# Kernel optimization log

Measured on AMD Instinct MI355X. Metric: run time of the kernel, lower is better.

The kernel has to match this reference:

```python
import jax, jax.numpy as jnp
import numpy as np

K = 16          # n_neighbors
DS = 4          # downsampling_rate
EPS = 1e-5      # BatchNorm eps


def fps(pos, n_samples):
    """Farthest point sampling. pos: [N,3] -> [n_samples] int32 indices (start at node 0)."""
    N = pos.shape[0]
    def body(carry, _):
        dists, last = carry
        d = jnp.sum((pos - pos[last]) ** 2, axis=-1)
        dists = jnp.minimum(dists, d)
        nxt = jnp.argmax(dists).astype(jnp.int32)
        return (dists, nxt), nxt
    init = (jnp.full((N,), 1e10, dtype=pos.dtype), jnp.int32(0))
    _, idxs = jax.lax.scan(body, init, None, length=n_samples - 1)
    return jnp.concatenate([jnp.zeros((1,), jnp.int32), idxs])


def knn(pos, k):
    """k nearest neighbors (incl. self). pos: [N,3] -> [N,k] indices."""
    d = jnp.sum((pos[:, None, :] - pos[None, :, :]) ** 2, axis=-1)  # [N,N]
    _, idx = jax.lax.top_k(-d, k)
    return idx


def setup_inputs() -> dict:
    key = jax.random.key(0)
    ks = jax.random.split(key, 8)
    B, N, C = 4, 4096, 64
    sizes = [C + 3, 128, 128]
    inp = {
        "feat": jax.random.normal(ks[0], (B, N, C), jnp.float32),
        "pos": jax.random.normal(ks[1], (B, N, 3), jnp.float32),
    }
    for i in range(2):
        cin, cout = sizes[i], sizes[i + 1]
        inp[f"W{i+1}"] = jax.random.normal(ks[2 + 2 * i], (cout, cin), jnp.float32) / np.float32(np.sqrt(cin))
        inp[f"b{i+1}"] = jnp.zeros((cout,), jnp.float32)
        inp[f"gamma{i+1}"] = jnp.ones((cout,), jnp.float32)
        inp[f"beta{i+1}"] = jnp.zeros((cout,), jnp.float32)
    return inp


def reference(feat, pos, W1, b1, gamma1, beta1, W2, b2, gamma2, beta2):
    B, N, C = feat.shape
    n_samples = N // DS
    # FPS centroids; the torch code selects them via a boolean mask, i.e. ascending node order
    cent = jax.vmap(lambda p: fps(p, n_samples))(pos)          # [B,S]
    cent = jnp.sort(cent, axis=-1)
    # KNN graph per cloud
    nbr = jax.vmap(lambda p: knn(p, K))(pos)                    # [B,N,K]
    nbr_pos = jax.vmap(lambda p, i: p[i])(pos, nbr)             # [B,N,K,3]
    nbr_feat = jax.vmap(lambda f, i: f[i])(feat, nbr)           # [B,N,K,C]
    # RelativePositionMessage: concat(src_pos - dst_pos, src_feat)
    rel = nbr_pos - pos[:, :, None, :]
    h = jnp.concatenate([rel, nbr_feat], axis=-1)               # [B,N,K,C+3]
    # PointNetConv: (1x1 Conv2d -> BatchNorm2d(training stats) -> ReLU) x2, then max over neighbors
    for W, b, g, be in ((W1, b1, gamma1, beta1), (W2, b2, gamma2, beta2)):
        h = jnp.einsum('bnkc,dc->bnkd', h, W) + b
        mu = jnp.mean(h, axis=(0, 1, 2))
        var = jnp.var(h, axis=(0, 1, 2))
        h = (h - mu) * jax.lax.rsqrt(var + EPS) * g + be
        h = jax.nn.relu(h)
    new_feat = jnp.max(h, axis=2)                               # [B,N,Cout]
    # select centroid nodes
    pos_res = jnp.take_along_axis(pos, cent[..., None], axis=1)        # [B,S,3]
    feat_res = jnp.take_along_axis(new_feat, cent[..., None], axis=1)  # [B,S,Cout]
    return pos_res, feat_res
```

## Files before the change

### kernel.cpp

```cpp
#include <hip/hip_runtime.h>

#define NB 4
#define NN 4096
#define NC 64
#define KNB 16
#define NS 1024
#define M1TOT (NB*NN*KNB)
#define EPSBN 1e-5f
#define XROW 68

__device__ __align__(16) int   g_nbr[NB*NN*KNB];
__device__ int   g_cslot[NB*NN];
__device__ float g_sum1[128];
__device__ float g_sq1[128];
__device__ float g_sum2[128];
__device__ float g_sq2[128];
__device__ __align__(16) float g_hmin[NB*NS*128];
__device__ __align__(16) float g_hmax[NB*NS*128];

__global__ __launch_bounds__(256) void kA(const float* __restrict__ pos, float* __restrict__ out)
{
    __shared__ float spx[NN], spy[NN], spz[NN];
    __shared__ float sbv[2][4];
    __shared__ int   sbj[2][4];
    __shared__ int   cnts[256];
    const int blk = blockIdx.x, t = threadIdx.x;

    if (blk >= 68) {
        if (t < 128) { g_sum1[t]=0.f; g_sq1[t]=0.f; g_sum2[t]=0.f; g_sq2[t]=0.f; }
        return;
    }

    if (blk < 4) {
        const int b = blk;
        const float* pb = pos + (size_t)b*NN*3;
        for (int i = t; i < NN; i += 256) { spx[i]=pb[3*i]; spy[i]=pb[3*i+1]; spz[i]=pb[3*i+2]; }
        __syncthreads();
        float rx[16], ry[16], rz[16], rd[16];
        #pragma unroll
        for (int i=0;i<16;i++){ int j=(t<<4)+i; rx[i]=spx[j]; ry[i]=spy[j]; rz[i]=spz[j]; rd[i]=1e10f; }
        unsigned sel = (t==0) ? 1u : 0u;
        float cx = spx[0], cy = spy[0], cz = spz[0];
        const int lane = t & 63, wid = t >> 6;

        for (int it = 0; it < NS-1; ++it) {
            const int par = it & 1;
            float bv = -1.f; int bj = 0;
            #pragma unroll
            for (int i=0;i<16;i++){
                float dx = rx[i]-cx, dy = ry[i]-cy, dz = rz[i]-cz;
                float d = __fadd_rn(__fadd_rn(__fmul_rn(dx,dx),__fmul_rn(dy,dy)),__fmul_rn(dz,dz));
                float nd = fminf(rd[i], d);
                rd[i] = nd;
                if (nd > bv) { bv = nd; bj = (t<<4)+i; }
            }
            #pragma unroll
            for (int m=1;m<64;m<<=1){
                float ov = __shfl_xor(bv, m);
                int   oj = __shfl_xor(bj, m);
                if (ov > bv || (ov == bv && oj < bj)) { bv = ov; bj = oj; }
            }
            if (lane == 0) { sbv[par][wid] = bv; sbj[par][wid] = bj; }
            __syncthreads();
            float v2 = sbv[par][lane & 3];
            int   j2 = sbj[par][lane & 3];
            #pragma unroll
            for (int m=1;m<4;m<<=1){
                float ov = __shfl_xor(v2, m);
                int   oj = __shfl_xor(j2, m);
                if (ov > v2 || (ov == v2 && oj < j2)) { v2 = ov; j2 = oj; }
            }
            cx = spx[j2]; cy = spy[j2]; cz = spz[j2];
            unsigned rel = (unsigned)(j2 - (t<<4));
            if (rel < 16u) sel |= (1u << rel);
        }
        cnts[t] = (int)__popc(sel);
        __syncthreads();
        if (t == 0) { int run = 0; for (int i=0;i<256;i++){ int c = cnts[i]; cnts[i] = run; run += c; } }
        __syncthreads();
        int base = cnts[t];
        #pragma unroll
        for (int i=0;i<16;i++){
            int j = (t<<4)+i;
            if (sel & (1u<<i)) {
                g_cslot[b*NN + j] = base;
                float* po = out + (size_t)((b<<10) + base)*3;
                po[0]=rx[i]; po[1]=ry[i]; po[2]=rz[i];
                base++;
            } else {
                g_cslot[b*NN + j] = -1;
            }
        }
    } else {
        const int kb = blk - 4;
        const int b = kb >> 4;
        const int q = ((kb & 15) << 8) + t;
        const float* pb = pos + (size_t)b*NN*3;
        for (int i = t; i < NN; i += 256) { spx[i]=pb[3*i]; spy[i]=pb[3*i+1]; spz[i]=pb[3*i+2]; }
        __syncthreads();
        const float qx = spx[q], qy = spy[q], qz = spz[q];
        float bd[16]; int bi[16];
        #pragma unroll
        for (int u=0;u<16;u++){ bd[u]=3e38f; bi[u]=0; }
        float wmax = 3e38f;
        for (int j = 0; j < NN; ++j) {
            float dx = spx[j]-qx, dy = spy[j]-qy, dz = spz[j]-qz;
            float d = __fadd_rn(__fadd_rn(__fmul_rn(dx,dx),__fmul_rn(dy,dy)),__fmul_rn(dz,dz));
            if (d < wmax) {
                float m0 = bd[0]; int mj = 0;
                #pragma unroll
                for (int u=1;u<16;u++){ if (bd[u] > m0) { m0 = bd[u]; mj = u; } }
                #pragma unroll
                for (int u=0;u<16;u++){ if (u == mj) { bd[u] = d; bi[u] = j; } }
                wmax = bd[0];
                #pragma unroll
                for (int u=1;u<16;u++) wmax = fmaxf(wmax, bd[u]);
            }
        }
        int* dst = g_nbr + ((size_t)(b*NN + q) << 4);
        #pragma unroll
        for (int u=0;u<16;u++) dst[u] = bi[u];
    }
}

__device__ __forceinline__ void stage_gemm1(const float* __restrict__ feat, const float* __restrict__ pos,
                                            const float* __restrict__ W1,
                                            float* __restrict__ xls, float* __restrict__ wls,
                                            int b, int nb, int t, float acc[4][8])
{
    for (int i = t; i < 128*67; i += 256) {
        int co = i / 67, ci = i - co*67;
        int row = (ci < 3) ? (64 + ci) : (ci - 3);
        wls[row*128 + co] = W1[i];
    }
    {
        const int s = t >> 2, h = t & 3;
        const int n = nb + (s >> 4), k = s & 15;
        const int gq = b*NN + n;
        const int idx = g_nbr[(gq << 4) + k];
        const float* fr = feat + ((size_t)(b*NN + idx) << 6) + (h << 4);
        float* xr = xls + s*XROW + (h << 4);
        #pragma unroll
        for (int u=0;u<4;u++) ((float4*)xr)[u] = ((const float4*)fr)[u];
        if (h == 0) {
            const float* pn = pos + (size_t)gq*3;
            const float* pi = pos + (size_t)(b*NN + idx)*3;
            xls[s*XROW + 64] = pi[0]-pn[0];
            xls[s*XROW + 65] = pi[1]-pn[1];
            xls[s*XROW + 66] = pi[2]-pn[2];
        }
    }
    __syncthreads();
    const int cg = t & 15, sg = t >> 4;
    #pragma unroll
    for (int r=0;r<4;r++)
        #pragma unroll
        for (int c=0;c<8;c++) acc[r][c] = 0.f;
    for (int i = 0; i < 67; ++i) {
        float4 wa = *(const float4*)&wls[i*128 + (cg<<3)];
        float4 wb = *(const float4*)&wls[i*128 + (cg<<3) + 4];
        #pragma unroll
        for (int r=0;r<4;r++){
            float xv = xls[(sg + (r<<4))*XROW + i];
            acc[r][0] = fmaf(xv, wa.x, acc[r][0]);
            acc[r][1] = fmaf(xv, wa.y, acc[r][1]);
            acc[r][2] = fmaf(xv, wa.z, acc[r][2]);
            acc[r][3] = fmaf(xv, wa.w, acc[r][3]);
            acc[r][4] = fmaf(xv, wb.x, acc[r][4]);
            acc[r][5] = fmaf(xv, wb.y, acc[r][5]);
            acc[r][6] = fmaf(xv, wb.z, acc[r][6]);
            acc[r][7] = fmaf(xv, wb.w, acc[r][7]);
        }
    }
}

__global__ __launch_bounds__(256) void kStats1(const float* __restrict__ feat, const float* __restrict__ pos,
                                               const float* __restrict__ W1, const float* __restrict__ b1)
{
    __shared__ __align__(16) float xls[64*XROW];
    __shared__ __align__(16) float wls[67*128];
    __shared__ float redS4[512], redQ4[512];
    const int t = threadIdx.x, blk = blockIdx.x;
    const int b = blk >> 10, nb = (blk & 1023) << 2;
    float acc[4][8];
    stage_gemm1(feat, pos, W1, xls, wls, b, nb, t, acc);
    const int cg = t & 15, sg = t >> 4, w = sg >> 2;
    #pragma unroll
    for (int c=0;c<8;c++){
        const int ch = (cg<<3)+c;
        const float bb = b1[ch];
        float ls=0.f, lq=0.f;
        #pragma unroll
        for (int r=0;r<4;r++){ float h1 = acc[r][c] + bb; ls += h1; lq = fmaf(h1,h1,lq); }
        ls += __shfl_xor(ls,16); ls += __shfl_xor(ls,32);
        lq += __shfl_xor(lq,16); lq += __shfl_xor(lq,32);
        if ((sg & 3) == 0) { redS4[w*128 + ch] = ls; redQ4[w*128 + ch] = lq; }
    }
    __syncthreads();
    if (t < 128) {
        float s = redS4[t] + redS4[128+t] + redS4[256+t] + redS4[384+t];
        float q = redQ4[t] + redQ4[128+t] + redQ4[256+t] + redQ4[384+t];
        atomicAdd(&g_sum1[t], s);
        atomicAdd(&g_sq1[t], q);
    }
}

__global__ __launch_bounds__(256) void kPassB(const float* __restrict__ feat, const float* __restrict__ pos,
        const float* __restrict__ W1, const float* __restrict__ b1,
        const float* __restrict__ gamma1, const float* __restrict__ beta1,
        const float* __restrict__ W2, const float* __restrict__ b2)
{
    __shared__ __align__(16) float SB[12928];
    __shared__ float scs[128], shs[128];
    __shared__ float redS4[512], redQ4[512];
    const int t = threadIdx.x, blk = blockIdx.x;
    const int b = blk >> 10, nb = (blk & 1023) << 2;
    if (t < 128) {
        const float inv = 1.f/(float)M1TOT;
        float mu  = g_sum1[t]*inv;
        float var = g_sq1[t]*inv - mu*mu;
        float sc  = gamma1[t]*rsqrtf(var + EPSBN);
        scs[t] = sc; shs[t] = beta1[t] - mu*sc;
    }
    float acc[4][8];
    stage_gemm1(feat, pos, W1, SB, SB + 64*XROW, b, nb, t, acc);
    const int cg = t & 15, sg = t >> 4, w = sg >> 2;
    __syncthreads();
    #pragma unroll
    for (int c=0;c<8;c++){
        const int ch = (cg<<3)+c;
        const float bb = b1[ch], sc = scs[ch], sh = shs[ch];
        #pragma unroll
        for (int r=0;r<4;r++){
            float yv = fmaxf(0.f, fmaf(acc[r][c] + bb, sc, sh));
            SB[(sg + (r<<4))*133 + ch] = yv;
        }
    }
    __syncthreads();
    float acc2[4][8];
    #pragma unroll
    for (int r=0;r<4;r++)
        #pragma unroll
        for (int c=0;c<8;c++) acc2[r][c]=0.f;
    for (int kc = 0; kc < 4; ++kc) {
        for (int e = t; e < 4096; e += 256) {
            int dd = e >> 5, kk = e & 31;
            SB[8512 + kk*128 + dd] = W2[(dd << 7) + (kc<<5) + kk];
        }
        __syncthreads();
        for (int kk = 0; kk < 32; ++kk) {
            float4 wa = *(const float4*)&SB[8512 + (kk<<7) + (cg<<3)];
            float4 wb = *(const float4*)&SB[8512 + (kk<<7) + (cg<<3) + 4];
            const int kabs = (kc<<5) + kk;
            #pragma unroll
            for (int r=0;r<4;r++){
                float yv = SB[((sg<<2) + r)*133 + kabs];
                acc2[r][0] = fmaf(yv, wa.x, acc2[r][0]);
                acc2[r][1] = fmaf(yv, wa.y, acc2[r][1]);
                acc2[r][2] = fmaf(yv, wa.z, acc2[r][2]);
                acc2[r][3] = fmaf(yv, wa.w, acc2[r][3]);
                acc2[r][4] = fmaf(yv, wb.x, acc2[r][4]);
                acc2[r][5] = fmaf(yv, wb.y, acc2[r][5]);
                acc2[r][6] = fmaf(yv, wb.z, acc2[r][6]);
                acc2[r][7] = fmaf(yv, wb.w, acc2[r][7]);
            }
        }
        __syncthreads();
    }
    #pragma unroll
    for (int c=0;c<8;c++){
        const int ch = (cg<<3)+c;
        const float bb = b2[ch];
        float ls=0.f, lq=0.f, mn=3e38f, mx=-3e38f;
        #pragma unroll
        for (int r=0;r<4;r++){
            float h2 = acc2[r][c] + bb;
            ls += h2; lq = fmaf(h2,h2,lq);
            mn = fminf(mn,h2); mx = fmaxf(mx,h2);
        }
        ls += __shfl_xor(ls,16); ls += __shfl_xor(ls,32);
        lq += __shfl_xor(lq,16); lq += __shfl_xor(lq,32);
        if ((sg & 3) == 0) { redS4[w*128 + ch] = ls; redQ4[w*128 + ch] = lq; }
        float o;
        o = __shfl_xor(mn,16); mn = fminf(mn,o);
        o = __shfl_xor(mn,32); mn = fminf(mn,o);
        o = __shfl_xor(mx,16); mx = fmaxf(mx,o);
        o = __shfl_xor(mx,32); mx = fmaxf(mx,o);
        if ((sg & 3) == 0) {
            const int node = nb + (sg >> 2);
            const int slot = g_cslot[b*NN + node];
            if (slot >= 0) {
                const int oo = (((b<<10)+slot)<<7) + ch;
                g_hmin[oo] = mn; g_hmax[oo] = mx;
            }
        }
    }
    __syncthreads();
    if (t < 128) {
        float s = redS4[t] + redS4[128+t] + redS4[256+t] + redS4[384+t];
        float q = redQ4[t] + redQ4[128+t] + redQ4[256+t] + redQ4[384+t];
        atomicAdd(&g_sum2[t], s);
        atomicAdd(&g_sq2[t], q);
    }
}

__global__ __launch_bounds__(256) void kFinal(const float* __restrict__ gamma2, const float* __restrict__ beta2,
                                              float* __restrict__ out)
{
    const int gid = blockIdx.x*256 + threadIdx.x;
    const int base = gid << 2;
    const int ch0 = base & 127;
    const float inv = 1.f/(float)M1TOT;
    float4 mx = *(const float4*)&g_hmax[base];
    float4 mn = *(const float4*)&g_hmin[base];
    float4 o;
    {
        float mu = g_sum2[ch0]*inv, var = g_sq2[ch0]*inv - mu*mu;
        float sc = gamma2[ch0]*rsqrtf(var+EPSBN), sh = beta2[ch0] - mu*sc;
        o.x = fmaxf(0.f, fmaf((sc >= 0.f) ? mx.x : mn.x, sc, sh));
    }
    {
        int ch = ch0+1;
        float mu = g_sum2[ch]*inv, var = g_sq2[ch]*inv - mu*mu;
        float sc = gamma2[ch]*rsqrtf(var+EPSBN), sh = beta2[ch] - mu*sc;
        o.y = fmaxf(0.f, fmaf((sc >= 0.f) ? mx.y : mn.y, sc, sh));
    }
    {
        int ch = ch0+2;
        float mu = g_sum2[ch]*inv, var = g_sq2[ch]*inv - mu*mu;
        float sc = gamma2[ch]*rsqrtf(var+EPSBN), sh = beta2[ch] - mu*sc;
        o.z = fmaxf(0.f, fmaf((sc >= 0.f) ? mx.z : mn.z, sc, sh));
    }
    {
        int ch = ch0+3;
        float mu = g_sum2[ch]*inv, var = g_sq2[ch]*inv - mu*mu;
        float sc = gamma2[ch]*rsqrtf(var+EPSBN), sh = beta2[ch] - mu*sc;
        o.w = fmaxf(0.f, fmaf((sc >= 0.f) ? mx.w : mn.w, sc, sh));
    }
    *(float4*)&out[12288 + base] = o;
}

extern "C" void kernel_launch(void* const* d_in, const int* in_sizes, int n_in,
                              void* d_out, int out_size, void* d_ws, size_t ws_size,
                              hipStream_t stream)
{
    (void)in_sizes; (void)n_in; (void)d_ws; (void)ws_size; (void)out_size;
    const float* feat = (const float*)d_in[0];
    const float* pos  = (const float*)d_in[1];
    const float* W1   = (const float*)d_in[2];
    const float* b1   = (const float*)d_in[3];
    const float* g1   = (const float*)d_in[4];
    const float* be1  = (const float*)d_in[5];
    const float* W2   = (const float*)d_in[6];
    const float* b2   = (const float*)d_in[7];
    const float* g2   = (const float*)d_in[8];
    const float* be2  = (const float*)d_in[9];
    float* out = (float*)d_out;

    kA<<<dim3(69),   dim3(256), 0, stream>>>(pos, out);
    kStats1<<<dim3(4096), dim3(256), 0, stream>>>(feat, pos, W1, b1);
    kPassB<<<dim3(4096),  dim3(256), 0, stream>>>(feat, pos, W1, b1, g1, be1, W2, b2);
    kFinal<<<dim3(512),   dim3(256), 0, stream>>>(g2, be2, out);
}
```

Measured before the change: 1.783 ms.

## Split FPS across kernels to overlap with GEMM stages and store h1

Farthest point sampling is split into three chunks whose state is kept in global memory, and each chunk runs in four extra blocks of the KNN kernel and the two GEMM kernels, so the serial FPS loop overlaps with other work. The first-layer activations are written to a large global buffer (g_h1) so the second pass reads them back instead of redoing the gather and GEMM1. Per-node min and max are now stored for every node and picked by centroid index in the final kernel. FPS and KNN use packed float2 math, KNN handles two queries per thread, and the GEMM weights are laid out for float4 loads. The cost is much more global memory traffic for h1 and the per-node min/max, plus a few long-running FPS blocks inside the GEMM grids.

```diff
diff --git a/kernel.cpp b/kernel.cpp
--- a/kernel.cpp
+++ b/kernel.cpp
@@ -1,242 +1,346 @@
 #include <hip/hip_runtime.h>
+
+typedef float f2 __attribute__((ext_vector_type(2)));
 
 #define NB 4
 #define NN 4096
-#define NC 64
 #define KNB 16
 #define NS 1024
 #define M1TOT (NB*NN*KNB)
 #define EPSBN 1e-5f
-#define XROW 68
-
+#define FPS_E0 255
+#define FPS_E1 639
+
+__device__ __align__(16) float g_h1[M1TOT*128];
 __device__ __align__(16) int   g_nbr[NB*NN*KNB];
-__device__ int   g_cslot[NB*NN];
-__device__ float g_sum1[128];
-__device__ float g_sq1[128];
-__device__ float g_sum2[128];
-__device__ float g_sq2[128];
-__device__ __align__(16) float g_hmin[NB*NS*128];
-__device__ __align__(16) float g_hmax[NB*NS*128];
-
-__global__ __launch_bounds__(256) void kA(const float* __restrict__ pos, float* __restrict__ out)
-{
-    __shared__ float spx[NN], spy[NN], spz[NN];
-    __shared__ float sbv[2][4];
-    __shared__ int   sbj[2][4];
-    __shared__ int   cnts[256];
-    const int blk = blockIdx.x, t = threadIdx.x;
-
-    if (blk >= 68) {
-        if (t < 128) { g_sum1[t]=0.f; g_sq1[t]=0.f; g_sum2[t]=0.f; g_sq2[t]=0.f; }
-        return;
-    }
-
-    if (blk < 4) {
-        const int b = blk;
-        const float* pb = pos + (size_t)b*NN*3;
-        for (int i = t; i < NN; i += 256) { spx[i]=pb[3*i]; spy[i]=pb[3*i+1]; spz[i]=pb[3*i+2]; }
+__device__ __align__(16) float g_fps_rd[NB][NN];
+__device__ unsigned g_fps_sel[NB][256];
+__device__ int   g_fps_last[NB];
+__device__ int   g_cent[NB][NS];
+__device__ float g_sum1[128], g_sq1[128], g_sum2[128], g_sq2[128];
+__device__ __align__(16) float g_hminN[NB*NN*128];
+__device__ __align__(16) float g_hmaxN[NB*NN*128];
+
+struct __align__(16) FpsSm {
+    float spx[NN], spy[NN], spz[NN];
+    float sv[2][4]; int sj[2][4];
+    int   cnts[256];
+};
+struct __align__(16) G1Sm {
+    float  xls[64*68];
+    float4 wlsA[68*16], wlsB[68*16];
+    float  redS[512], redQ[512];
+};
+struct __align__(16) G2Sm {
+    float  yls[64*132];
+    float4 w2A[32*16], w2B[32*16];
+    float  scs[128], shs[128];
+    float  redS[512], redQ[512];
+};
+
+__device__ __forceinline__ void fps_chunk(const float* __restrict__ pos, float* __restrict__ out,
+                                          FpsSm* sm, int b, int t, int it0, int it1,
+                                          bool first, bool last)
+{
+#pragma clang fp contract(off)
+    const float* pb = pos + b*NN*3;
+    for (int i = t; i < NN; i += 256) { sm->spx[i]=pb[3*i]; sm->spy[i]=pb[3*i+1]; sm->spz[i]=pb[3*i+2]; }
+    __syncthreads();
+    f2 rx[8], ry[8], rz[8], rd[8];
+    #pragma unroll
+    for (int p=0;p<8;p++){
+        int j = (t<<4) + 2*p;
+        rx[p] = (f2){sm->spx[j], sm->spx[j+1]};
+        ry[p] = (f2){sm->spy[j], sm->spy[j+1]};
+        rz[p] = (f2){sm->spz[j], sm->spz[j+1]};
+    }
+    unsigned sel; int j2;
+    if (first) {
+        #pragma unroll
+        for (int p=0;p<8;p++) rd[p] = (f2){1e10f, 1e10f};
+        sel = (t==0) ? 1u : 0u;
+        j2 = 0;
+    } else {
+        #pragma unroll
+        for (int u=0;u<4;u++){
+            float4 ld = *(const float4*)&g_fps_rd[b][(t<<4)+(u<<2)];
+            rd[2*u]   = (f2){ld.x, ld.y};
+            rd[2*u+1] = (f2){ld.z, ld.w};
+        }
+        sel = g_fps_sel[b][t];
+        j2  = g_fps_last[b];
+    }
+    float cx = sm->spx[j2], cy = sm->spy[j2], cz = sm->spz[j2];
+    const int lane = t & 63, wid = t >> 6;
+
+    for (int it = it0; it < it1; ++it) {
+        const int par = it & 1;
+        f2 c2x = {cx,cx}, c2y = {cy,cy}, c2z = {cz,cz};
+        f2 bv2 = {-1.f,-1.f};
+        #pragma unroll
+        for (int p=0;p<8;p++){
+            f2 dx = rx[p]-c2x, dy = ry[p]-c2y, dz = rz[p]-c2z;
+            f2 m0 = dx*dx, m1 = dy*dy, m2 = dz*dz;
+            f2 a0 = m0 + m1;
+            f2 d  = a0 + m2;
+            rd[p] = __builtin_elementwise_min(rd[p], d);
+            bv2   = __builtin_elementwise_max(bv2, rd[p]);
+        }
+        float bv = fmaxf(bv2.x, bv2.y);
+        int bj = 0;
+        #pragma unroll
+        for (int p=7;p>=0;p--){
+            bj = (rd[p].y == bv) ? ((t<<4)+2*p+1) : bj;
+            bj = (rd[p].x == bv) ? ((t<<4)+2*p)   : bj;
+        }
+        #pragma unroll
+        for (int m=1;m<64;m<<=1){
+            float ov = __shfl_xor(bv, m);
+            int   oj = __shfl_xor(bj, m);
+            if (ov > bv || (ov == bv && oj < bj)) { bv = ov; bj = oj; }
+        }
+        if (lane == 0) { sm->sv[par][wid] = bv; sm->sj[par][wid] = bj; }
         __syncthreads();
-        float rx[16], ry[16], rz[16], rd[16];
-        #pragma unroll
-        for (int i=0;i<16;i++){ int j=(t<<4)+i; rx[i]=spx[j]; ry[i]=spy[j]; rz[i]=spz[j]; rd[i]=1e10f; }
-        unsigned sel = (t==0) ? 1u : 0u;
-        float cx = spx[0], cy = spy[0], cz = spz[0];
-        const int lane = t & 63, wid = t >> 6;
-
-        for (int it = 0; it < NS-1; ++it) {
-            const int par = it & 1;
-            float bv = -1.f; int bj = 0;
-            #pragma unroll
-            for (int i=0;i<16;i++){
-                float dx = rx[i]-cx, dy = ry[i]-cy, dz = rz[i]-cz;
-                float d = __fadd_rn(__fadd_rn(__fmul_rn(dx,dx),__fmul_rn(dy,dy)),__fmul_rn(dz,dz));
-                float nd = fminf(rd[i], d);
-                rd[i] = nd;
-                if (nd > bv) { bv = nd; bj = (t<<4)+i; }
-            }
-            #pragma unroll
-            for (int m=1;m<64;m<<=1){
-                float ov = __shfl_xor(bv, m);
-                int   oj = __shfl_xor(bj, m);
-                if (ov > bv || (ov == bv && oj < bj)) { bv = ov; bj = oj; }
-            }
-            if (lane == 0) { sbv[par][wid] = bv; sbj[par][wid] = bj; }
-            __syncthreads();
-            float v2 = sbv[par][lane & 3];
-            int   j2 = sbj[par][lane & 3];
-            #pragma unroll
-            for (int m=1;m<4;m<<=1){
-                float ov = __shfl_xor(v2, m);
-                int   oj = __shfl_xor(j2, m);
-                if (ov > v2 || (ov == v2 && oj < j2)) { v2 = ov; j2 = oj; }
-            }
-            cx = spx[j2]; cy = spy[j2]; cz = spz[j2];
-            unsigned rel = (unsigned)(j2 - (t<<4));
-            if (rel < 16u) sel |= (1u << rel);
-        }
-        cnts[t] = (int)__popc(sel);
+        float v = sm->sv[par][0]; int jn = sm->sj[par][0];
+        #pragma unroll
+        for (int w=1;w<4;w++){
+            float ov = sm->sv[par][w]; int oj = sm->sj[par][w];
+            if (ov > v || (ov == v && oj < jn)) { v = ov; jn = oj; }
+        }
+        j2 = jn;
+        cx = sm->spx[j2]; cy = sm->spy[j2]; cz = sm->spz[j2];
+        unsigned rel = (unsigned)(j2 - (t<<4));
+        if (rel < 16u) sel |= (1u << rel);
+    }
+
+    if (!last) {
+        #pragma unroll
+        for (int u=0;u<4;u++){
+            float4 st = {rd[2*u].x, rd[2*u].y, rd[2*u+1].x, rd[2*u+1].y};
+            *(float4*)&g_fps_rd[b][(t<<4)+(u<<2)] = st;
+        }
+        g_fps_sel[b][t] = sel;
+        if (t == 0) g_fps_last[b] = j2;
+    } else {
+        sm->cnts[t] = (int)__popc(sel);
         __syncthreads();
-        if (t == 0) { int run = 0; for (int i=0;i<256;i++){ int c = cnts[i]; cnts[i] = run; run += c; } }
+        if (t == 0) { int run = 0; for (int i=0;i<256;i++){ int c = sm->cnts[i]; sm->cnts[i] = run; run += c; } }
         __syncthreads();
-        int base = cnts[t];
+        int base = sm->cnts[t];
         #pragma unroll
         for (int i=0;i<16;i++){
             int j = (t<<4)+i;
             if (sel & (1u<<i)) {
-                g_cslot[b*NN + j] = base;
-                float* po = out + (size_t)((b<<10) + base)*3;
-                po[0]=rx[i]; po[1]=ry[i]; po[2]=rz[i];
+                g_cent[b][base] = j;
+                float* po = out + (size_t)((b<<10)+base)*3;
+                po[0]=sm->spx[j]; po[1]=sm->spy[j]; po[2]=sm->spz[j];
                 base++;
-            } else {
-                g_cslot[b*NN + j] = -1;
             }
         }
-    } else {
-        const int kb = blk - 4;
-        const int b = kb >> 4;
-        const int q = ((kb & 15) << 8) + t;
-        const float* pb = pos + (size_t)b*NN*3;
-        for (int i = t; i < NN; i += 256) { spx[i]=pb[3*i]; spy[i]=pb[3*i+1]; spz[i]=pb[3*i+2]; }
-        __syncthreads();
-        const float qx = spx[q], qy = spy[q], qz = spz[q];
-        float bd[16]; int bi[16];
-        #pragma unroll
-        for (int u=0;u<16;u++){ bd[u]=3e38f; bi[u]=0; }
-        float wmax = 3e38f;
-        for (int j = 0; j < NN; ++j) {
-            float dx = spx[j]-qx, dy = spy[j]-qy, dz = spz[j]-qz;
-            float d = __fadd_rn(__fadd_rn(__fmul_rn(dx,dx),__fmul_rn(dy,dy)),__fmul_rn(dz,dz));
-            if (d < wmax) {
-                float m0 = bd[0]; int mj = 0;
-                #pragma unroll
-                for (int u=1;u<16;u++){ if (bd[u] > m0) { m0 = bd[u]; mj = u; } }
-                #pragma unroll
-                for (int u=0;u<16;u++){ if (u == mj) { bd[u] = d; bi[u] = j; } }
-                wmax = bd[0];
-                #pragma unroll
-                for (int u=1;u<16;u++) wmax = fmaxf(wmax, bd[u]);
-            }
-        }
-        int* dst = g_nbr + ((size_t)(b*NN + q) << 4);
-        #pragma unroll
-        for (int u=0;u<16;u++) dst[u] = bi[u];
-    }
-}
-
-__device__ __forceinline__ void stage_gemm1(const float* __restrict__ feat, const float* __restrict__ pos,
-                                            const float* __restrict__ W1,
-                                            float* __restrict__ xls, float* __restrict__ wls,
-                                            int b, int nb, int t, float acc[4][8])
-{
-    for (int i = t; i < 128*67; i += 256) {
-        int co = i / 67, ci = i - co*67;
+    }
+}
+
+__device__ __forceinline__ void knn_ins(float (&bd)[16], int (&bi)[16], float &wmax, float d, int j)
+{
+    float m0 = bd[0]; int mj = 0;
+    #pragma unroll
+    for (int u=1;u<16;u++){ if (bd[u] > m0){ m0 = bd[u]; mj = u; } }
+    #pragma unroll
+    for (int u=0;u<16;u++){ if (u == mj){ bd[u] = d; bi[u] = j; } }
+    float w = bd[0];
+    #pragma unroll
+    for (int u=1;u<16;u++) w = fmaxf(w, bd[u]);
+    wmax = w;
+}
+
+__global__ __launch_bounds__(256) void kPre(const float* __restrict__ pos)
+{
+#pragma clang fp contract(off)
+    __shared__ FpsSm sm;
+    const int blk = blockIdx.x, t = threadIdx.x;
+    if (blk >= 36) {
+        if (t < 128) { g_sum1[t]=0.f; g_sq1[t]=0.f; g_sum2[t]=0.f; g_sq2[t]=0.f; }
+        return;
+    }
+    if (blk < 4) {
+        fps_chunk(pos, nullptr, &sm, blk, t, 0, FPS_E0, true, false);
+        return;
+    }
+    const int kb = blk - 4;
+    const int b = kb >> 3;
+    const int q0 = ((kb & 7) << 9) + t;
+    const int q1 = q0 + 256;
+    const float* pb = pos + b*NN*3;
+    for (int i = t; i < NN; i += 256) { sm.spx[i]=pb[3*i]; sm.spy[i]=pb[3*i+1]; sm.spz[i]=pb[3*i+2]; }
+    __syncthreads();
+    const float qx0=sm.spx[q0], qy0=sm.spy[q0], qz0=sm.spz[q0];
+    const float qx1=sm.spx[q1], qy1=sm.spy[q1], qz1=sm.spz[q1];
+    float bd0[16], bd1[16]; int bi0[16], bi1[16];
+    #pragma unroll
+    for (int u=0;u<16;u++){ bd0[u]=3e38f; bi0[u]=0; bd1[u]=3e38f; bi1[u]=0; }
+    float wm0 = 3e38f, wm1 = 3e38f;
+    const f2 v0x={qx0,qx0}, v0y={qy0,qy0}, v0z={qz0,qz0};
+    const f2 v1x={qx1,qx1}, v1y={qy1,qy1}, v1z={qz1,qz1};
+    for (int j = 0; j < NN; j += 2) {
+        f2 px = *(const f2*)&sm.spx[j];
+        f2 py = *(const f2*)&sm.spy[j];
+        f2 pz = *(const f2*)&sm.spz[j];
+        {
+            f2 dx = px - v0x, dy = py - v0y, dz = pz - v0z;
+            f2 m0 = dx*dx, m1 = dy*dy, m2 = dz*dz;
+            f2 a0 = m0 + m1; f2 d = a0 + m2;
+            if (d.x < wm0) knn_ins(bd0, bi0, wm0, d.x, j);
+            if (d.y < wm0) knn_ins(bd0, bi0, wm0, d.y, j+1);
+        }
+        {
+            f2 dx = px - v1x, dy = py - v1y, dz = pz - v1z;
+            f2 m0 = dx*dx, m1 = dy*dy, m2 = dz*dz;
+            f2 a0 = m0 + m1; f2 d = a0 + m2;
+            if (d.x < wm1) knn_ins(bd1, bi1, wm1, d.x, j);
+            if (d.y < wm1) knn_ins(bd1, bi1, wm1, d.y, j+1);
+        }
+    }
+    int* dst0 = g_nbr + ((size_t)(b*NN + q0) << 4);
+    int* dst1 = g_nbr + ((size_t)(b*NN + q1) << 4);
+    #pragma unroll
+    for (int u=0;u<16;u++){ dst0[u] = bi0[u]; dst1[u] = bi1[u]; }
+}
+
+__global__ __launch_bounds__(256) void kS1(const float* __restrict__ feat, const float* __restrict__ pos,
+                                           const float* __restrict__ W1, const float* __restrict__ b1)
+{
+    __shared__ union { FpsSm f; G1Sm g; } sm;
+    const int blk = blockIdx.x, t = threadIdx.x;
+    if (blk < 4) { fps_chunk(pos, nullptr, &sm.f, blk, t, FPS_E0, FPS_E1, false, false); return; }
+    const int gb = blk - 4;
+    const int b = gb >> 10, nb = (gb & 1023) << 2;
+
+    for (int e = t; e < 128*67; e += 256) {
+        int co = e / 67, ci = e - co*67;
         int row = (ci < 3) ? (64 + ci) : (ci - 3);
-        wls[row*128 + co] = W1[i];
-    }
+        int cgd = co >> 3, h = co & 7;
+        float w = W1[e];
+        if (h < 4) ((float*)&sm.g.wlsA[row*16 + cgd])[h]   = w;
+        else       ((float*)&sm.g.wlsB[row*16 + cgd])[h-4] = w;
+    }
+    if (t < 64) { ((float*)&sm.g.wlsA[67*16])[t] = 0.f; ((float*)&sm.g.wlsB[67*16])[t] = 0.f; }
     {
         const int s = t >> 2, h = t & 3;
         const int n = nb + (s >> 4), k = s & 15;
         const int gq = b*NN + n;
         const int idx = g_nbr[(gq << 4) + k];
         const float* fr = feat + ((size_t)(b*NN + idx) << 6) + (h << 4);
-        float* xr = xls + s*XROW + (h << 4);
+        float* xr = sm.g.xls + s*68 + (h << 4);
         #pragma unroll
         for (int u=0;u<4;u++) ((float4*)xr)[u] = ((const float4*)fr)[u];
         if (h == 0) {
             const float* pn = pos + (size_t)gq*3;
             const float* pi = pos + (size_t)(b*NN + idx)*3;
-            xls[s*XROW + 64] = pi[0]-pn[0];
-            xls[s*XROW + 65] = pi[1]-pn[1];
-            xls[s*XROW + 66] = pi[2]-pn[2];
-        }
-    }
-    __syncthreads();
-    const int cg = t & 15, sg = t >> 4;
+            sm.g.xls[s*68 + 64] = pi[0]-pn[0];
+            sm.g.xls[s*68 + 65] = pi[1]-pn[1];
+            sm.g.xls[s*68 + 66] = pi[2]-pn[2];
+            sm.g.xls[s*68 + 67] = 0.f;
+        }
+    }
+    __syncthreads();
+    const int cg = t & 15, sg = t >> 4, w = t >> 6;
+    float acc[4][8];
     #pragma unroll
     for (int r=0;r<4;r++)
         #pragma unroll
         for (int c=0;c<8;c++) acc[r][c] = 0.f;
-    for (int i = 0; i < 67; ++i) {
-        float4 wa = *(const float4*)&wls[i*128 + (cg<<3)];
-        float4 wb = *(const float4*)&wls[i*128 + (cg<<3) + 4];
+    for (int c4 = 0; c4 < 17; ++c4) {
+        float4 wA[4], wB[4];
+        #pragma unroll
+        for (int ii=0;ii<4;ii++){ wA[ii] = sm.g.wlsA[(4*c4+ii)*16 + cg]; wB[ii] = sm.g.wlsB[(4*c4+ii)*16 + cg]; }
         #pragma unroll
         for (int r=0;r<4;r++){
-            float xv = xls[(sg + (r<<4))*XROW + i];
-            acc[r][0] = fmaf(xv, wa.x, acc[r][0]);
-            acc[r][1] = fmaf(xv, wa.y, acc[r][1]);
-            acc[r][2] = fmaf(xv, wa.z, acc[r][2]);
-            acc[r][3] = fmaf(xv, wa.w, acc[r][3]);
-            acc[r][4] = fmaf(xv, wb.x, acc[r][4]);
-            acc[r][5] = fmaf(xv, wb.y, acc[r][5]);
-            acc[r][6] = fmaf(xv, wb.z, acc[r][6]);
-            acc[r][7] = fmaf(xv, wb.w, acc[r][7]);
-        }
-    }
-}
-
-__global__ __launch_bounds__(256) void kStats1(const float* __restrict__ feat, const float* __restrict__ pos,
-                                               const float* __restrict__ W1, const float* __restrict__ b1)
-{
-    __shared__ __align__(16) float xls[64*XROW];
-    __shared__ __align__(16) float wls[67*128];
-    __shared__ float redS4[512], redQ4[512];
-    const int t = threadIdx.x, blk = blockIdx.x;
-    const int b = blk >> 10, nb = (blk & 1023) << 2;
-    float acc[4][8];
-    stage_gemm1(feat, pos, W1, xls, wls, b, nb, t, acc);
-    const int cg = t & 15, sg = t >> 4, w = sg >> 2;
+            float4 xv = *(const float4*)&sm.g.xls[(sg + (r<<4))*68 + (c4<<2)];
+            #pragma unroll
+            for (int ii=0;ii<4;ii++){
+                float x = (ii==0)?xv.x:(ii==1)?xv.y:(ii==2)?xv.z:xv.w;
+                acc[r][0] = fmaf(x, wA[ii].x, acc[r][0]);
+                acc[r][1] = fmaf(x, wA[ii].y, acc[r][1]);
+                acc[r][2] = fmaf(x, wA[ii].z, acc[r][2]);
+                acc[r][3] = fmaf(x, wA[ii].w, acc[r][3]);
+                acc[r][4] = fmaf(x, wB[ii].x, acc[r][4]);
+                acc[r][5] = fmaf(x, wB[ii].y, acc[r][5]);
+                acc[r][6] = fmaf(x, wB[ii].z, acc[r][6]);
+                acc[r][7] = fmaf(x, wB[ii].w, acc[r][7]);
+            }
+        }
+    }
+    float4 bA = *(const float4*)&b1[cg<<3];
+    float4 bB = *(const float4*)&b1[(cg<<3)+4];
+    float h1v[4][8];
+    #pragma unroll
+    for (int r=0;r<4;r++){
+        h1v[r][0]=acc[r][0]+bA.x; h1v[r][1]=acc[r][1]+bA.y; h1v[r][2]=acc[r][2]+bA.z; h1v[r][3]=acc[r][3]+bA.w;
+        h1v[r][4]=acc[r][4]+bB.x; h1v[r][5]=acc[r][5]+bB.y; h1v[r][6]=acc[r][6]+bB.z; h1v[r][7]=acc[r][7]+bB.w;
+    }
     #pragma unroll
     for (int c=0;c<8;c++){
         const int ch = (cg<<3)+c;
-        const float bb = b1[ch];
         float ls=0.f, lq=0.f;
         #pragma unroll
-        for (int r=0;r<4;r++){ float h1 = acc[r][c] + bb; ls += h1; lq = fmaf(h1,h1,lq); }
+        for (int r=0;r<4;r++){ float h1 = h1v[r][c]; ls += h1; lq = fmaf(h1,h1,lq); }
         ls += __shfl_xor(ls,16); ls += __shfl_xor(ls,32);
         lq += __shfl_xor(lq,16); lq += __shfl_xor(lq,32);
-        if ((sg & 3) == 0) { redS4[w*128 + ch] = ls; redQ4[w*128 + ch] = lq; }
+        if ((sg & 3) == 0) { sm.g.redS[w*128 + ch] = ls; sm.g.redQ[w*128 + ch] = lq; }
+    }
+    #pragma unroll
+    for (int r=0;r<4;r++){
+        const int gs = (b*NN + nb + r)*16 + sg;
+        float4 o0 = {h1v[r][0],h1v[r][1],h1v[r][2],h1v[r][3]};
+        float4 o1 = {h1v[r][4],h1v[r][5],h1v[r][6],h1v[r][7]};
+        *(float4*)&g_h1[gs*128 + (cg<<3)]     = o0;
+        *(float4*)&g_h1[gs*128 + (cg<<3) + 4] = o1;
     }
     __syncthreads();
     if (t < 128) {
-        float s = redS4[t] + redS4[128+t] + redS4[256+t] + redS4[384+t];
-        float q = redQ4[t] + redQ4[128+t] + redQ4[256+t] + redQ4[384+t];
+        float s = sm.g.redS[t] + sm.g.redS[128+t] + sm.g.redS[256+t] + sm.g.redS[384+t];
+        float q = sm.g.redQ[t] + sm.g.redQ[128+t] + sm.g.redQ[256+t] + sm.g.redQ[384+t];
         atomicAdd(&g_sum1[t], s);
         atomicAdd(&g_sq1[t], q);
     }
 }
 
-__global__ __launch_bounds__(256) void kPassB(const float* __restrict__ feat, const float* __restrict__ pos,
-        const float* __restrict__ W1, const float* __restrict__ b1,
-        const float* __restrict__ gamma1, const float* __restrict__ beta1,
-        const float* __restrict__ W2, const float* __restrict__ b2)
-{
-    __shared__ __align__(16) float SB[12928];
-    __shared__ float scs[128], shs[128];
-    __shared__ float redS4[512], redQ4[512];
-    const int t = threadIdx.x, blk = blockIdx.x;
-    const int b = blk >> 10, nb = (blk & 1023) << 2;
+__global__ __launch_bounds__(256) void kS2(const float* __restrict__ pos, float* __restrict__ out,
+        const float* __restrict__ W2, const float* __restrict__ b2,
+        const float* __restrict__ gamma1, const float* __restrict__ beta1)
+{
+    __shared__ union { FpsSm f; G2Sm g; } sm;
+    const int blk = blockIdx.x, t = threadIdx.x;
+    if (blk < 4) { fps_chunk(pos, out, &sm.f, blk, t, FPS_E1, NS-1, false, true); return; }
+    const int gb = blk - 4;
+    const int b = gb >> 10, nb = (gb & 1023) << 2;
     if (t < 128) {
         const float inv = 1.f/(float)M1TOT;
         float mu  = g_sum1[t]*inv;
         float var = g_sq1[t]*inv - mu*mu;
         float sc  = gamma1[t]*rsqrtf(var + EPSBN);
-        scs[t] = sc; shs[t] = beta1[t] - mu*sc;
-    }
-    float acc[4][8];
-    stage_gemm1(feat, pos, W1, SB, SB + 64*XROW, b, nb, t, acc);
-    const int cg = t & 15, sg = t >> 4, w = sg >> 2;
-    __syncthreads();
-    #pragma unroll
-    for (int c=0;c<8;c++){
-        const int ch = (cg<<3)+c;
-        const float bb = b1[ch], sc = scs[ch], sh = shs[ch];
-        #pragma unroll
-        for (int r=0;r<4;r++){
-            float yv = fmaxf(0.f, fmaf(acc[r][c] + bb, sc, sh));
-            SB[(sg + (r<<4))*133 + ch] = yv;
-        }
-    }
-    __syncthreads();
+        sm.g.scs[t] = sc; sm.g.shs[t] = beta1[t] - mu*sc;
+    }
+    __syncthreads();
+    {
+        const float* hsrc = g_h1 + (size_t)((b*NN + nb)*16)*128;
+        const int ch0 = (4*t) & 127;
+        float4 sc4 = *(const float4*)&sm.g.scs[ch0];
+        float4 sh4 = *(const float4*)&sm.g.shs[ch0];
+        #pragma unroll
+        for (int j=0;j<8;j++){
+            int f = j*1024 + 4*t;
+            float4 v = *(const float4*)&hsrc[f];
+            int s = f >> 7;
+            float4 yv;
+            yv.x = fmaxf(0.f, fmaf(v.x, sc4.x, sh4.x));
+            yv.y = fmaxf(0.f, fmaf(v.y, sc4.y, sh4.y));
+            yv.z = fmaxf(0.f, fmaf(v.z, sc4.z, sh4.z));
+            yv.w = fmaxf(0.f, fmaf(v.w, sc4.w, sh4.w));
+            *(float4*)&sm.g.yls[s*132 + ch0] = yv;
+        }
+    }
+    const int cg = t & 15, sg = t >> 4, w = t >> 6;
     float acc2[4][8];
     #pragma unroll
     for (int r=0;r<4;r++)
@@ -244,29 +348,38 @@
         for (int c=0;c<8;c++) acc2[r][c]=0.f;
     for (int kc = 0; kc < 4; ++kc) {
         for (int e = t; e < 4096; e += 256) {
-            int dd = e >> 5, kk = e & 31;
-            SB[8512 + kk*128 + dd] = W2[(dd << 7) + (kc<<5) + kk];
+            int d = e >> 5, kk = e & 31;
+            float wv = W2[(d << 7) + (kc<<5) + kk];
+            int cgd = d >> 3, h = d & 7;
+            if (h < 4) ((float*)&sm.g.w2A[kk*16 + cgd])[h]   = wv;
+            else       ((float*)&sm.g.w2B[kk*16 + cgd])[h-4] = wv;
         }
         __syncthreads();
-        for (int kk = 0; kk < 32; ++kk) {
-            float4 wa = *(const float4*)&SB[8512 + (kk<<7) + (cg<<3)];
-            float4 wb = *(const float4*)&SB[8512 + (kk<<7) + (cg<<3) + 4];
-            const int kabs = (kc<<5) + kk;
+        #pragma unroll
+        for (int c4=0;c4<8;c4++){
+            float4 wA[4], wB[4];
+            #pragma unroll
+            for (int ii=0;ii<4;ii++){ wA[ii] = sm.g.w2A[(4*c4+ii)*16 + cg]; wB[ii] = sm.g.w2B[(4*c4+ii)*16 + cg]; }
             #pragma unroll
             for (int r=0;r<4;r++){
-                float yv = SB[((sg<<2) + r)*133 + kabs];
-                acc2[r][0] = fmaf(yv, wa.x, acc2[r][0]);
-                acc2[r][1] = fmaf(yv, wa.y, acc2[r][1]);
-                acc2[r][2] = fmaf(yv, wa.z, acc2[r][2]);
-                acc2[r][3] = fmaf(yv, wa.w, acc2[r][3]);
-                acc2[r][4] = fmaf(yv, wb.x, acc2[r][4]);
-                acc2[r][5] = fmaf(yv, wb.y, acc2[r][5]);
-                acc2[r][6] = fmaf(yv, wb.z, acc2[r][6]);
-                acc2[r][7] = fmaf(yv, wb.w, acc2[r][7]);
+                float4 yv = *(const float4*)&sm.g.yls[((sg<<2)+r)*132 + (kc<<5) + (c4<<2)];
+                #pragma unroll
+                for (int ii=0;ii<4;ii++){
+                    float y = (ii==0)?yv.x:(ii==1)?yv.y:(ii==2)?yv.z:yv.w;
+                    acc2[r][0] = fmaf(y, wA[ii].x, acc2[r][0]);
+                    acc2[r][1] = fmaf(y, wA[ii].y, acc2[r][1]);
+                    acc2[r][2] = fmaf(y, wA[ii].z, acc2[r][2]);
+                    acc2[r][3] = fmaf(y, wA[ii].w, acc2[r][3]);
+                    acc2[r][4] = fmaf(y, wB[ii].x, acc2[r][4]);
+                    acc2[r][5] = fmaf(y, wB[ii].y, acc2[r][5]);
+                    acc2[r][6] = fmaf(y, wB[ii].z, acc2[r][6]);
+                    acc2[r][7] = fmaf(y, wB[ii].w, acc2[r][7]);
+                }
             }
         }
         __syncthreads();
     }
+    const int node = nb + (sg >> 2);
     #pragma unroll
     for (int c=0;c<8;c++){
         const int ch = (cg<<3)+c;
@@ -280,25 +393,21 @@
         }
         ls += __shfl_xor(ls,16); ls += __shfl_xor(ls,32);
         lq += __shfl_xor(lq,16); lq += __shfl_xor(lq,32);
-        if ((sg & 3) == 0) { redS4[w*128 + ch] = ls; redQ4[w*128 + ch] = lq; }
+        if ((sg & 3) == 0) { sm.g.redS[w*128 + ch] = ls; sm.g.redQ[w*128 + ch] = lq; }
         float o;
         o = __shfl_xor(mn,16); mn = fminf(mn,o);
         o = __shfl_xor(mn,32); mn = fminf(mn,o);
         o = __shfl_xor(mx,16); mx = fmaxf(mx,o);
         o = __shfl_xor(mx,32); mx = fmaxf(mx,o);
         if ((sg & 3) == 0) {
-            const int node = nb + (sg >> 2);
-            const int slot = g_cslot[b*NN + node];
-            if (slot >= 0) {
-                const int oo = (((b<<10)+slot)<<7) + ch;
-                g_hmin[oo] = mn; g_hmax[oo] = mx;
-            }
+            const int oo = ((b<<12)+node)*128 + ch;
+            g_hminN[oo] = mn; g_hmaxN[oo] = mx;
         }
     }
     __syncthreads();
     if (t < 128) {
-        float s = redS4[t] + redS4[128+t] + redS4[256+t] + redS4[384+t];
-        float q = redQ4[t] + redQ4[128+t] + redQ4[256+t] + redQ4[384+t];
+        float s = sm.g.redS[t] + sm.g.redS[128+t] + sm.g.redS[256+t] + sm.g.redS[384+t];
+        float q = sm.g.redQ[t] + sm.g.redQ[128+t] + sm.g.redQ[256+t] + sm.g.redQ[384+t];
         atomicAdd(&g_sum2[t], s);
         atomicAdd(&g_sq2[t], q);
     }
@@ -309,33 +418,24 @@
 {
     const int gid = blockIdx.x*256 + threadIdx.x;
     const int base = gid << 2;
+    const int sl = base >> 7;
+    const int b = sl >> 10, slot = sl & 1023;
     const int ch0 = base & 127;
+    const int node = g_cent[b][slot];
+    const int src = ((b<<12)+node)*128 + ch0;
     const float inv = 1.f/(float)M1TOT;
-    float4 mx = *(const float4*)&g_hmax[base];
-    float4 mn = *(const float4*)&g_hmin[base];
+    float4 mx = *(const float4*)&g_hmaxN[src];
+    float4 mn = *(const float4*)&g_hminN[src];
     float4 o;
-    {
-        float mu = g_sum2[ch0]*inv, var = g_sq2[ch0]*inv - mu*mu;
-        float sc = gamma2[ch0]*rsqrtf(var+EPSBN), sh = beta2[ch0] - mu*sc;
-        o.x = fmaxf(0.f, fmaf((sc >= 0.f) ? mx.x : mn.x, sc, sh));
-    }
-    {
-        int ch = ch0+1;
+    #pragma unroll
+    for (int c=0;c<4;c++){
+        int ch = ch0 + c;
         float mu = g_sum2[ch]*inv, var = g_sq2[ch]*inv - mu*mu;
         float sc = gamma2[ch]*rsqrtf(var+EPSBN), sh = beta2[ch] - mu*sc;
-        o.y = fmaxf(0.f, fmaf((sc >= 0.f) ? mx.y : mn.y, sc, sh));
-    }
-    {
-        int ch = ch0+2;
-        float mu = g_sum2[ch]*inv, var = g_sq2[ch]*inv - mu*mu;
-        float sc = gamma2[ch]*rsqrtf(var+EPSBN), sh = beta2[ch] - mu*sc;
-        o.z = fmaxf(0.f, fmaf((sc >= 0.f) ? mx.z : mn.z, sc, sh));
-    }
-    {
-        int ch = ch0+3;
-        float mu = g_sum2[ch]*inv, var = g_sq2[ch]*inv - mu*mu;
-        float sc = gamma2[ch]*rsqrtf(var+EPSBN), sh = beta2[ch] - mu*sc;
-        o.w = fmaxf(0.f, fmaf((sc >= 0.f) ? mx.w : mn.w, sc, sh));
+        float hi = (c==0)?mx.x:(c==1)?mx.y:(c==2)?mx.z:mx.w;
+        float lo = (c==0)?mn.x:(c==1)?mn.y:(c==2)?mn.z:mn.w;
+        float v = fmaxf(0.f, fmaf((sc >= 0.f) ? hi : lo, sc, sh));
+        if (c==0) o.x=v; else if (c==1) o.y=v; else if (c==2) o.z=v; else o.w=v;
     }
     *(float4*)&out[12288 + base] = o;
 }
@@ -357,8 +457,8 @@
     const float* be2  = (const float*)d_in[9];
     float* out = (float*)d_out;
 
-    kA<<<dim3(69),   dim3(256), 0, stream>>>(pos, out);
-    kStats1<<<dim3(4096), dim3(256), 0, stream>>>(feat, pos, W1, b1);
-    kPassB<<<dim3(4096),  dim3(256), 0, stream>>>(feat, pos, W1, b1, g1, be1, W2, b2);
-    kFinal<<<dim3(512),   dim3(256), 0, stream>>>(g2, be2, out);
-}
+    kPre  <<<dim3(37),   dim3(256), 0, stream>>>(pos);
+    kS1   <<<dim3(4100), dim3(256), 0, stream>>>(feat, pos, W1, b1);
+    kS2   <<<dim3(4100), dim3(256), 0, stream>>>(pos, out, W2, b2, g1, be1);
+    kFinal<<<dim3(512),  dim3(256), 0, stream>>>(g2, be2, out);
+}
```

Result: slower. 4.135 ms (+132.0%).
